# Kernel tuning notes

Hardware: AMD Instinct MI355X
Metric: run time of the kernel (lower is better)

Reference implementation:

```python
import jax, jax.numpy as jnp
import numpy as np

B, T, DIN, DOUT, RANK, UDIM = 4, 2048, 4096, 4096, 2, 16

def setup_inputs() -> dict:
    key = jax.random.key(0)
    ks = jax.random.split(key, 8)
    return {
        "x": jax.random.normal(ks[0], (B, T, DIN), jnp.float32),
        "W": jax.random.normal(ks[1], (DOUT, DIN), jnp.float32) * 0.02,
        "b": jax.random.normal(ks[2], (DOUT,), jnp.float32) * 0.02,
        "U": jax.random.normal(ks[3], (DOUT, RANK), jnp.float32) * 0.02,
        "S": jax.random.normal(ks[4], (RANK, RANK), jnp.float32),
        "Vh": jax.random.normal(ks[5], (RANK, DIN), jnp.float32) * 0.02,
        "P": jax.random.normal(ks[6], (UDIM, RANK, RANK), jnp.float32),
        "v": jax.random.normal(ks[7], (UDIM,), jnp.float32),
    }

def reference(x, W, b, U, S, Vh, P, v):
    # R = sum_u v[u] * P[u]  (intended meaning of einsum('u,urr->rr'))
    R = jnp.einsum('u,uab->ab', v, P)                 # [rank, rank]
    base = jnp.einsum('btd,od->bto', x, W) + b        # frozen linear
    # x @ delta_W.T with delta_W = U @ S @ R @ Vh, chained low-rank:
    M = U @ S @ R                                     # [out, rank]
    t = jnp.einsum('btd,rd->btr', x, Vh)              # [B, T, rank]
    delta = jnp.einsum('btr,or->bto', t, M)           # [B, T, out]
    return base + delta
```

## Files before the change

kernel.cpp:

```cpp
#include <hip/hip_runtime.h>
#include <hip/hip_bf16.h>
#include <stdint.h>

typedef __hip_bfloat16 bf16;
typedef __attribute__((ext_vector_type(8))) short bf16x8;
typedef __attribute__((ext_vector_type(4))) float f32x4;

static constexpr int Mtot = 8192;
static constexpr int Ktot = 4096;
static constexpr int Ntot = 4096;
static constexpr int BM = 256, BN = 256, BK = 64;
static constexpr int NKT = Ktot / BK;
static constexpr int CAST_BLOCKS = (Mtot * Ktot) / 2048;
static constexpr int PREP_BLOCKS = (Ntot * Ktot) / 2048;
static constexpr int WEFF_BLOCKS = Ntot * 2;

__device__ __forceinline__ void gl_lds16(const void* g, void* l) {
  __builtin_amdgcn_global_load_lds(
      (const __attribute__((address_space(1))) void*)g,
      (__attribute__((address_space(3))) void*)l,
      16, 0, 0);
}

__device__ __forceinline__ uint32_t bf16pair(float a, float b) {
  __hip_bfloat16 ha = __float2bfloat16(a), hb = __float2bfloat16(b);
  uint16_t ia, ib;
  __builtin_memcpy(&ia, &ha, 2);
  __builtin_memcpy(&ib, &hb, 2);
  return (uint32_t)ia | ((uint32_t)ib << 16);
}

__global__ __launch_bounds__(256) void mprep_kernel(const float* __restrict__ U,
                                                    const float* __restrict__ S,
                                                    const float* __restrict__ P,
                                                    const float* __restrict__ v,
                                                    float* __restrict__ M) {
  float R0 = 0.f, R1 = 0.f, R2 = 0.f, R3 = 0.f;
#pragma unroll
  for (int u = 0; u < 16; ++u) {
    float vu = v[u];
    R0 += vu * P[u * 4 + 0];
    R1 += vu * P[u * 4 + 1];
    R2 += vu * P[u * 4 + 2];
    R3 += vu * P[u * 4 + 3];
  }
  float SR00 = S[0] * R0 + S[1] * R2, SR01 = S[0] * R1 + S[1] * R3;
  float SR10 = S[2] * R0 + S[3] * R2, SR11 = S[2] * R1 + S[3] * R3;
  const int o = blockIdx.x * 256 + threadIdx.x;
  const float u0 = U[o * 2 + 0], u1 = U[o * 2 + 1];
  ((float2*)M)[o] = make_float2(u0 * SR00 + u1 * SR10, u0 * SR01 + u1 * SR11);
}

__global__ __launch_bounds__(256) void prep_kernel(const float* __restrict__ x,
                                                   bf16* __restrict__ xb,
                                                   const float* __restrict__ W,
                                                   const float* __restrict__ Vh,
                                                   const float* __restrict__ M,
                                                   bf16* __restrict__ Wp) {
  const int bid = blockIdx.x;
  const int t = threadIdx.x;
  if (bid < CAST_BLOCKS) {
    const size_t chunk = (size_t)bid * 2048;
    const float4 a = *(const float4*)(x + chunk + 4 * t);
    const float4 b = *(const float4*)(x + chunk + 1024 + 4 * t);
    uint2 p0, p1;
    p0.x = bf16pair(a.x, a.y); p0.y = bf16pair(a.z, a.w);
    p1.x = bf16pair(b.x, b.y); p1.y = bf16pair(b.z, b.w);
    *(uint2*)(xb + chunk + 4 * t) = p0;
    *(uint2*)(xb + chunk + 1024 + 4 * t) = p1;
  } else {
    const int b2 = bid - CAST_BLOCKS;
    const int o = b2 >> 1;
    const int cb = (b2 & 1) * 2048 + 4 * t;
    const float2 Mo = ((const float2*)M)[o];

    const float* wrow = W + (size_t)o * Ktot;
    const float4 w0 = *(const float4*)(wrow + cb);
    const float4 w1 = *(const float4*)(wrow + cb + 1024);
    const float4 a0 = *(const float4*)(Vh + cb);
    const float4 a1 = *(const float4*)(Vh + cb + 1024);
    const float4 b0 = *(const float4*)(Vh + Ktot + cb);
    const float4 b1 = *(const float4*)(Vh + Ktot + cb + 1024);

    uint2 p0, p1;
    p0.x = bf16pair(w0.x + Mo.x * a0.x + Mo.y * b0.x,
                    w0.y + Mo.x * a0.y + Mo.y * b0.y);
    p0.y = bf16pair(w0.z + Mo.x * a0.z + Mo.y * b0.z,
                    w0.w + Mo.x * a0.w + Mo.y * b0.w);
    p1.x = bf16pair(w1.x + Mo.x * a1.x + Mo.y * b1.x,
                    w1.y + Mo.x * a1.y + Mo.y * b1.y);
    p1.y = bf16pair(w1.z + Mo.x * a1.z + Mo.y * b1.z,
                    w1.w + Mo.x * a1.w + Mo.y * b1.w);
    *(uint2*)(Wp + (size_t)o * Ktot + cb) = p0;
    *(uint2*)(Wp + (size_t)o * Ktot + cb + 1024) = p1;
  }
}


#define SCHEDB __builtin_amdgcn_sched_barrier(0)
#define BAR do { SCHEDB; __builtin_amdgcn_s_barrier(); SCHEDB; } while (0)
#define LG0 do { asm volatile("s_waitcnt lgkmcnt(0)" ::: "memory"); SCHEDB; } while (0)
#define LG8 do { asm volatile("s_waitcnt lgkmcnt(8)" ::: "memory"); } while (0)
#define WVM(n) do { asm volatile("s_waitcnt vmcnt(" #n ")" ::: "memory"); } while (0)

__global__ __launch_bounds__(512, 2) void gemm_kernel(const bf16* __restrict__ A,
                                                      const bf16* __restrict__ Bt,
                                                      const float* __restrict__ bias,
                                                      float* __restrict__ out) {
  __shared__ __align__(16) bf16 As[2][BM * BK];
  __shared__ __align__(16) bf16 Bs[2][BN * BK];

  const int tid = (int)threadIdx.x;
  const int lane = tid & 63;
  const int w = tid >> 6;
  const int wr = w >> 2;
  const int wc = w & 3;

  const int bid = (int)blockIdx.x;
  const int xcd = bid & 7;
  const int ord = bid >> 3;
  const int rnd = ord >> 5;
  const int slt = ord & 31;
  const int mt = rnd * 16 + (xcd >> 1) * 4 + (slt >> 3);
  const int nt = (xcd & 1) * 8 + (slt & 7);
  const int m0 = mt * BM;
  const int n0 = nt * BN;

  const int l8 = lane >> 3;
  const int swcol = ((lane & 7) ^ l8) << 3;
  const bf16* gA = A + (size_t)(m0 + w * 16 + l8) * Ktot + swcol;
  const bf16* gB = Bt + (size_t)(n0 + w * 16 + l8) * Ktot + swcol;

  const int fm = lane & 15;
  const int q = lane >> 4;
  const int rx = (fm & 7) << 4;
  const int clo = (q * 16) ^ (rx & 48);
  const int aoff0 = (wr * 128 + fm) * 128 + clo + (rx & 64);
  const int aoff1 = (wr * 128 + fm) * 128 + clo + (64 ^ (rx & 64));
  const int boff0 = (wc * 64 + fm) * 128 + clo + (rx & 64);
  const int boff1 = (wc * 64 + fm) * 128 + clo + (64 ^ (rx & 64));

#define STA(BUF, half, kt) do { \
    const bf16* _g = gA + (size_t)((half) * 128) * Ktot + (kt) * 64; \
    char* _l = (char*)(&As[BUF][0]) + (half) * 16384 + w * 2048; \
    gl_lds16(_g, _l); \
    gl_lds16(_g + (size_t)8 * Ktot, _l + 1024); \
  } while (0)
#define STB(BUF, half, kt) do { \
    const bf16* _g = gB + (size_t)((half) * 128) * Ktot + (kt) * 64; \
    char* _l = (char*)(&Bs[BUF][0]) + (half) * 16384 + w * 2048; \
    gl_lds16(_g, _l); \
    gl_lds16(_g + (size_t)8 * Ktot, _l + 1024); \
  } while (0)
#define STAGE_H(BUF, h, kt) do { \
    if ((h) == 0) STA(BUF, 0, kt); else if ((h) == 1) STA(BUF, 1, kt); \
    else if ((h) == 2) STB(BUF, 0, kt); else STB(BUF, 1, kt); } while (0)

#define RD_A(dst, BUF, mh) do { \
    const char* _p = (const char*)(&As[BUF][0]) + (mh) * 8192; \
    _Pragma("unroll") for (int _i = 0; _i < 4; ++_i) { \
      dst[_i][0] = *(const bf16x8*)(_p + _i * 2048 + aoff0); \
      dst[_i][1] = *(const bf16x8*)(_p + _i * 2048 + aoff1); \
    } } while (0)
#define RD_B(dst, BUF, nh) do { \
    const char* _p = (const char*)(&Bs[BUF][0]) + (nh) * 4096; \
    _Pragma("unroll") for (int _j = 0; _j < 2; ++_j) { \
      dst[_j][0] = *(const bf16x8*)(_p + _j * 2048 + boff0); \
      dst[_j][1] = *(const bf16x8*)(_p + _j * 2048 + boff1); \
    } } while (0)

#define MFMA_Q(AV, BV, MH, NH) do { \
    __builtin_amdgcn_s_setprio(1); \
    _Pragma("unroll") for (int _i = 0; _i < 4; ++_i) \
    _Pragma("unroll") for (int _j = 0; _j < 2; ++_j) { \
      acc[(MH) * 4 + _i][(NH) * 2 + _j] = __builtin_amdgcn_mfma_f32_16x16x32_bf16( \
          AV[_i][0], BV[_j][0], acc[(MH) * 4 + _i][(NH) * 2 + _j], 0, 0, 0); \
      acc[(MH) * 4 + _i][(NH) * 2 + _j] = __builtin_amdgcn_mfma_f32_16x16x32_bf16( \
          AV[_i][1], BV[_j][1], acc[(MH) * 4 + _i][(NH) * 2 + _j], 0, 0, 0); \
    } \
    __builtin_amdgcn_s_setprio(0); \
  } while (0)

  f32x4 acc[8][4];
#pragma unroll
  for (int i = 0; i < 8; ++i)
#pragma unroll
    for (int j = 0; j < 4; ++j) acc[i][j] = {0.f, 0.f, 0.f, 0.f};

  bf16x8 a[4][2], b0[2][2], b1[2][2];

  STAGE_H(0, 0, 0); STAGE_H(0, 1, 0); STAGE_H(0, 2, 0); STAGE_H(0, 3, 0);
  STAGE_H(1, 2, 1); STAGE_H(1, 3, 1); STAGE_H(1, 0, 1);
  WVM(6);
  BAR;

  for (int it = 0; it < 31; ++it) {
    const int k1 = 2 * it + 1;
    const int k2 = 2 * it + 2;
    const int k3 = 2 * it + 3;
    RD_A(a, 0, 0); RD_B(b0, 0, 0); STAGE_H(1, 1, k1); LG8;
    BAR; LG0; MFMA_Q(a, b0, 0, 0); BAR;
    RD_B(b1, 0, 1);
    BAR; LG0; MFMA_Q(a, b1, 0, 1); BAR;
    RD_A(a, 0, 1); STAGE_H(0, 2, k2);
    BAR; LG0; MFMA_Q(a, b0, 1, 0); BAR;
    STAGE_H(0, 3, k2);
    BAR; MFMA_Q(a, b1, 1, 1); SCHEDB; WVM(4); BAR;
    RD_A(a, 1, 0); RD_B(b0, 1, 0); STAGE_H(0, 0, k2); LG8;
    BAR; LG0; MFMA_Q(a, b0, 0, 0); BAR;
    RD_B(b1, 1, 1); STAGE_H(0, 1, k2);
    BAR; LG0; MFMA_Q(a, b1, 0, 1); BAR;
    RD_A(a, 1, 1); STAGE_H(1, 2, k3);
    BAR; LG0; MFMA_Q(a, b0, 1, 0); BAR;
    STAGE_H(1, 3, k3); STAGE_H(1, 0, k3);
    BAR; MFMA_Q(a, b1, 1, 1); SCHEDB; WVM(6); BAR;
  }

  RD_A(a, 0, 0); RD_B(b0, 0, 0); STAGE_H(1, 1, 63); LG8;
  BAR; LG0; MFMA_Q(a, b0, 0, 0); BAR;
  RD_B(b1, 0, 1);
  BAR; LG0; MFMA_Q(a, b1, 0, 1); BAR;
  RD_A(a, 0, 1);
  BAR; LG0; MFMA_Q(a, b0, 1, 0); BAR;
  BAR; MFMA_Q(a, b1, 1, 1); SCHEDB; WVM(0); BAR;
  RD_A(a, 1, 0); RD_B(b0, 1, 0);
  BAR; LG0; MFMA_Q(a, b0, 0, 0); BAR;
  RD_B(b1, 1, 1);
  BAR; LG0; MFMA_Q(a, b1, 0, 1); BAR;
  RD_A(a, 1, 1);
  BAR; LG0; MFMA_Q(a, b0, 1, 0); BAR;
  MFMA_Q(a, b1, 1, 1);

#pragma unroll
  for (int jb = 0; jb < 4; ++jb) {
    const int gn = n0 + wc * 64 + jb * 16 + fm;
    const float bj = bias[gn];
#pragma unroll
    for (int ia = 0; ia < 8; ++ia) {
      float* o = out + (size_t)(m0 + wr * 128 + ia * 16 + q * 4) * Ntot + gn;
#pragma unroll
      for (int r = 0; r < 4; ++r) o[(size_t)r * Ntot] = acc[ia][jb][r] + bj;
    }
  }

#undef STA
#undef STB
#undef STAGE_H
#undef RD_A
#undef RD_B
#undef MFMA_Q
}

extern "C" void kernel_launch(void* const* d_in, const int* in_sizes, int n_in,
                              void* d_out, int out_size, void* d_ws, size_t ws_size,
                              hipStream_t stream) {
  const float* x  = (const float*)d_in[0];
  const float* W  = (const float*)d_in[1];
  const float* b  = (const float*)d_in[2];
  const float* U  = (const float*)d_in[3];
  const float* S  = (const float*)d_in[4];
  const float* Vh = (const float*)d_in[5];
  const float* P  = (const float*)d_in[6];
  const float* v  = (const float*)d_in[7];
  float* out = (float*)d_out;

  bf16* xb = (bf16*)d_ws;
  bf16* Wp = (bf16*)((char*)d_ws + (size_t)Mtot * Ktot * 2);
  float* M = out;

  mprep_kernel<<<16, 256, 0, stream>>>(U, S, P, v, M);
  prep_kernel<<<CAST_BLOCKS + WEFF_BLOCKS, 256, 0, stream>>>(x, xb, W, Vh, M, Wp);
  gemm_kernel<<<512, 512, 0, stream>>>(xb, Wp, b, out);
}
```

Before: 519.4 us.

## Fuse fp32-to-bf16 cast of x into GEMM A-tile staging

The separate pass that cast x to bf16 in workspace is removed. The GEMM now loads fp32 x tiles into registers, converts them to bf16 and writes them to swizzled LDS, with a reworked software pipeline and waitcnt schedule. This saves the extra global write and read of the bf16 copy of x (about 64MB of traffic). In exchange the GEMM reads twice as many A bytes per tile, A-staging now needs registers and VALU conversion work inside the main loop, and the direct global-to-LDS path is lost for A. The added register pressure could hurt occupancy, and the hand-tuned wait counts must be exactly right.

```diff
diff --git a/kernel.cpp b/kernel.cpp
--- a/kernel.cpp
+++ b/kernel.cpp
@@ -11,8 +11,6 @@
 static constexpr int Ntot = 4096;
 static constexpr int BM = 256, BN = 256, BK = 64;
 static constexpr int NKT = Ktot / BK;
-static constexpr int CAST_BLOCKS = (Mtot * Ktot) / 2048;
-static constexpr int PREP_BLOCKS = (Ntot * Ktot) / 2048;
 static constexpr int WEFF_BLOCKS = Ntot * 2;
 
 __device__ __forceinline__ void gl_lds16(const void* g, void* l) {
@@ -51,59 +49,45 @@
   ((float2*)M)[o] = make_float2(u0 * SR00 + u1 * SR10, u0 * SR01 + u1 * SR11);
 }
 
-__global__ __launch_bounds__(256) void prep_kernel(const float* __restrict__ x,
-                                                   bf16* __restrict__ xb,
-                                                   const float* __restrict__ W,
+__global__ __launch_bounds__(256) void prep_kernel(const float* __restrict__ W,
                                                    const float* __restrict__ Vh,
                                                    const float* __restrict__ M,
                                                    bf16* __restrict__ Wp) {
   const int bid = blockIdx.x;
   const int t = threadIdx.x;
-  if (bid < CAST_BLOCKS) {
-    const size_t chunk = (size_t)bid * 2048;
-    const float4 a = *(const float4*)(x + chunk + 4 * t);
-    const float4 b = *(const float4*)(x + chunk + 1024 + 4 * t);
-    uint2 p0, p1;
-    p0.x = bf16pair(a.x, a.y); p0.y = bf16pair(a.z, a.w);
-    p1.x = bf16pair(b.x, b.y); p1.y = bf16pair(b.z, b.w);
-    *(uint2*)(xb + chunk + 4 * t) = p0;
-    *(uint2*)(xb + chunk + 1024 + 4 * t) = p1;
-  } else {
-    const int b2 = bid - CAST_BLOCKS;
-    const int o = b2 >> 1;
-    const int cb = (b2 & 1) * 2048 + 4 * t;
-    const float2 Mo = ((const float2*)M)[o];
-
-    const float* wrow = W + (size_t)o * Ktot;
-    const float4 w0 = *(const float4*)(wrow + cb);
-    const float4 w1 = *(const float4*)(wrow + cb + 1024);
-    const float4 a0 = *(const float4*)(Vh + cb);
-    const float4 a1 = *(const float4*)(Vh + cb + 1024);
-    const float4 b0 = *(const float4*)(Vh + Ktot + cb);
-    const float4 b1 = *(const float4*)(Vh + Ktot + cb + 1024);
-
-    uint2 p0, p1;
-    p0.x = bf16pair(w0.x + Mo.x * a0.x + Mo.y * b0.x,
-                    w0.y + Mo.x * a0.y + Mo.y * b0.y);
-    p0.y = bf16pair(w0.z + Mo.x * a0.z + Mo.y * b0.z,
-                    w0.w + Mo.x * a0.w + Mo.y * b0.w);
-    p1.x = bf16pair(w1.x + Mo.x * a1.x + Mo.y * b1.x,
-                    w1.y + Mo.x * a1.y + Mo.y * b1.y);
-    p1.y = bf16pair(w1.z + Mo.x * a1.z + Mo.y * b1.z,
-                    w1.w + Mo.x * a1.w + Mo.y * b1.w);
-    *(uint2*)(Wp + (size_t)o * Ktot + cb) = p0;
-    *(uint2*)(Wp + (size_t)o * Ktot + cb + 1024) = p1;
-  }
+  const int o = bid >> 1;
+  const int cb = (bid & 1) * 2048 + 4 * t;
+  const float2 Mo = ((const float2*)M)[o];
+
+  const float* wrow = W + (size_t)o * Ktot;
+  const float4 w0 = *(const float4*)(wrow + cb);
+  const float4 w1 = *(const float4*)(wrow + cb + 1024);
+  const float4 a0 = *(const float4*)(Vh + cb);
+  const float4 a1 = *(const float4*)(Vh + cb + 1024);
+  const float4 b0 = *(const float4*)(Vh + Ktot + cb);
+  const float4 b1 = *(const float4*)(Vh + Ktot + cb + 1024);
+
+  uint2 p0, p1;
+  p0.x = bf16pair(w0.x + Mo.x * a0.x + Mo.y * b0.x,
+                  w0.y + Mo.x * a0.y + Mo.y * b0.y);
+  p0.y = bf16pair(w0.z + Mo.x * a0.z + Mo.y * b0.z,
+                  w0.w + Mo.x * a0.w + Mo.y * b0.w);
+  p1.x = bf16pair(w1.x + Mo.x * a1.x + Mo.y * b1.x,
+                  w1.y + Mo.x * a1.y + Mo.y * b1.y);
+  p1.y = bf16pair(w1.z + Mo.x * a1.z + Mo.y * b1.z,
+                  w1.w + Mo.x * a1.w + Mo.y * b1.w);
+  *(uint2*)(Wp + (size_t)o * Ktot + cb) = p0;
+  *(uint2*)(Wp + (size_t)o * Ktot + cb + 1024) = p1;
 }
 
 
 #define SCHEDB __builtin_amdgcn_sched_barrier(0)
 #define BAR do { SCHEDB; __builtin_amdgcn_s_barrier(); SCHEDB; } while (0)
 #define LG0 do { asm volatile("s_waitcnt lgkmcnt(0)" ::: "memory"); SCHEDB; } while (0)
-#define LG8 do { asm volatile("s_waitcnt lgkmcnt(8)" ::: "memory"); } while (0)
+#define LGN(n) do { asm volatile("s_waitcnt lgkmcnt(" #n ")" ::: "memory"); } while (0)
 #define WVM(n) do { asm volatile("s_waitcnt vmcnt(" #n ")" ::: "memory"); } while (0)
 
-__global__ __launch_bounds__(512, 2) void gemm_kernel(const bf16* __restrict__ A,
+__global__ __launch_bounds__(512, 2) void gemm_kernel(const float* __restrict__ x,
                                                       const bf16* __restrict__ Bt,
                                                       const float* __restrict__ bias,
                                                       float* __restrict__ out) {
@@ -128,8 +112,15 @@
 
   const int l8 = lane >> 3;
   const int swcol = ((lane & 7) ^ l8) << 3;
-  const bf16* gA = A + (size_t)(m0 + w * 16 + l8) * Ktot + swcol;
   const bf16* gB = Bt + (size_t)(n0 + w * 16 + l8) * Ktot + swcol;
+
+  const int ar = tid >> 2;
+  const int ac = (tid & 3) << 4;
+  const float* gAx = x + (size_t)(m0 + ar) * Ktot + ac;
+  const int c0 = (tid & 3) << 5;
+  const int asw = (ar & 7) << 4;
+  const int aw0 = ar * 128 + (c0 ^ asw);
+  const int aw1 = ar * 128 + ((c0 + 16) ^ asw);
 
   const int fm = lane & 15;
   const int q = lane >> 4;
@@ -140,11 +131,33 @@
   const int boff0 = (wc * 64 + fm) * 128 + clo + (rx & 64);
   const int boff1 = (wc * 64 + fm) * 128 + clo + (64 ^ (rx & 64));
 
-#define STA(BUF, half, kt) do { \
-    const bf16* _g = gA + (size_t)((half) * 128) * Ktot + (kt) * 64; \
-    char* _l = (char*)(&As[BUF][0]) + (half) * 16384 + w * 2048; \
-    gl_lds16(_g, _l); \
-    gl_lds16(_g + (size_t)8 * Ktot, _l + 1024); \
+#define IA0(ub, kt) do { \
+    const float* _g = gAx + (size_t)((ub) * 128) * Ktot + (kt) * 64; \
+    sA0[0] = *(const float4*)(_g + 0);  sA0[1] = *(const float4*)(_g + 4); \
+    sA0[2] = *(const float4*)(_g + 8);  sA0[3] = *(const float4*)(_g + 12); \
+  } while (0)
+#define IA1(ub, kt) do { \
+    const float* _g = gAx + (size_t)((ub) * 128) * Ktot + (kt) * 64; \
+    sA1[0] = *(const float4*)(_g + 0);  sA1[1] = *(const float4*)(_g + 4); \
+    sA1[2] = *(const float4*)(_g + 8);  sA1[3] = *(const float4*)(_g + 12); \
+  } while (0)
+#define WRA0(BUF, ub) do { \
+    char* _b = (char*)(&As[BUF][0]) + (ub) * 16384; \
+    uint4 _lo, _hi; \
+    _lo.x = bf16pair(sA0[0].x, sA0[0].y); _lo.y = bf16pair(sA0[0].z, sA0[0].w); \
+    _lo.z = bf16pair(sA0[1].x, sA0[1].y); _lo.w = bf16pair(sA0[1].z, sA0[1].w); \
+    _hi.x = bf16pair(sA0[2].x, sA0[2].y); _hi.y = bf16pair(sA0[2].z, sA0[2].w); \
+    _hi.z = bf16pair(sA0[3].x, sA0[3].y); _hi.w = bf16pair(sA0[3].z, sA0[3].w); \
+    *(uint4*)(_b + aw0) = _lo; *(uint4*)(_b + aw1) = _hi; \
+  } while (0)
+#define WRA1(BUF, ub) do { \
+    char* _b = (char*)(&As[BUF][0]) + (ub) * 16384; \
+    uint4 _lo, _hi; \
+    _lo.x = bf16pair(sA1[0].x, sA1[0].y); _lo.y = bf16pair(sA1[0].z, sA1[0].w); \
+    _lo.z = bf16pair(sA1[1].x, sA1[1].y); _lo.w = bf16pair(sA1[1].z, sA1[1].w); \
+    _hi.x = bf16pair(sA1[2].x, sA1[2].y); _hi.y = bf16pair(sA1[2].z, sA1[2].w); \
+    _hi.z = bf16pair(sA1[3].x, sA1[3].y); _hi.w = bf16pair(sA1[3].z, sA1[3].w); \
+    *(uint4*)(_b + aw0) = _lo; *(uint4*)(_b + aw1) = _hi; \
   } while (0)
 #define STB(BUF, half, kt) do { \
     const bf16* _g = gB + (size_t)((half) * 128) * Ktot + (kt) * 64; \
@@ -152,9 +165,6 @@
     gl_lds16(_g, _l); \
     gl_lds16(_g + (size_t)8 * Ktot, _l + 1024); \
   } while (0)
-#define STAGE_H(BUF, h, kt) do { \
-    if ((h) == 0) STA(BUF, 0, kt); else if ((h) == 1) STA(BUF, 1, kt); \
-    else if ((h) == 2) STB(BUF, 0, kt); else STB(BUF, 1, kt); } while (0)
 
 #define RD_A(dst, BUF, mh) do { \
     const char* _p = (const char*)(&As[BUF][0]) + (mh) * 8192; \
@@ -188,36 +198,50 @@
     for (int j = 0; j < 4; ++j) acc[i][j] = {0.f, 0.f, 0.f, 0.f};
 
   bf16x8 a[4][2], b0[2][2], b1[2][2];
-
-  STAGE_H(0, 0, 0); STAGE_H(0, 1, 0); STAGE_H(0, 2, 0); STAGE_H(0, 3, 0);
-  STAGE_H(1, 2, 1); STAGE_H(1, 3, 1); STAGE_H(1, 0, 1);
-  WVM(6);
+  float4 sA0[4], sA1[4];
+
+  IA0(0, 0); IA1(1, 0);
+  STB(0, 0, 0); STB(0, 1, 0);
+  WVM(8);  WRA0(0, 0);
+  WVM(4);  WRA1(0, 1);
+  IA0(0, 1);
+  WVM(0);  WRA0(1, 0);
+  IA1(1, 1);
+  STB(1, 0, 1); STB(1, 1, 1);
+  LGN(0);
   BAR;
 
   for (int it = 0; it < 31; ++it) {
-    const int k1 = 2 * it + 1;
     const int k2 = 2 * it + 2;
     const int k3 = 2 * it + 3;
-    RD_A(a, 0, 0); RD_B(b0, 0, 0); STAGE_H(1, 1, k1); LG8;
-    BAR; LG0; MFMA_Q(a, b0, 0, 0); BAR;
+    WVM(4); WRA1(1, 1);
+    RD_A(a, 0, 0); RD_B(b0, 0, 0);
+    LGN(12); BAR; LG0; MFMA_Q(a, b0, 0, 0); BAR;
     RD_B(b1, 0, 1);
     BAR; LG0; MFMA_Q(a, b1, 0, 1); BAR;
-    RD_A(a, 0, 1); STAGE_H(0, 2, k2);
+    IA0(0, k2); STB(0, 0, k2);
+    RD_A(a, 0, 1);
     BAR; LG0; MFMA_Q(a, b0, 1, 0); BAR;
-    STAGE_H(0, 3, k2);
-    BAR; MFMA_Q(a, b1, 1, 1); SCHEDB; WVM(4); BAR;
-    RD_A(a, 1, 0); RD_B(b0, 1, 0); STAGE_H(0, 0, k2); LG8;
-    BAR; LG0; MFMA_Q(a, b0, 0, 0); BAR;
-    RD_B(b1, 1, 1); STAGE_H(0, 1, k2);
-    BAR; LG0; MFMA_Q(a, b1, 0, 1); BAR;
-    RD_A(a, 1, 1); STAGE_H(1, 2, k3);
+    IA1(1, k2); STB(0, 1, k2);
+    BAR; MFMA_Q(a, b1, 1, 1); SCHEDB; WVM(12); BAR;
+    WVM(8); WRA0(0, 0);
+    RD_A(a, 1, 0); RD_B(b0, 1, 0);
+    LGN(12); BAR; LG0; MFMA_Q(a, b0, 0, 0); BAR;
+    IA0(0, k3);
+    WVM(6); WRA1(0, 1);
+    RD_B(b1, 1, 1);
+    LGN(4); BAR; LG0; MFMA_Q(a, b1, 0, 1); BAR;
+    IA1(1, k3); STB(1, 0, k3);
+    RD_A(a, 1, 1);
     BAR; LG0; MFMA_Q(a, b0, 1, 0); BAR;
-    STAGE_H(1, 3, k3); STAGE_H(1, 0, k3);
-    BAR; MFMA_Q(a, b1, 1, 1); SCHEDB; WVM(6); BAR;
+    STB(1, 1, k3);
+    WVM(8); WRA0(1, 0);
+    LGN(0); BAR; MFMA_Q(a, b1, 1, 1); BAR;
   }
 
-  RD_A(a, 0, 0); RD_B(b0, 0, 0); STAGE_H(1, 1, 63); LG8;
-  BAR; LG0; MFMA_Q(a, b0, 0, 0); BAR;
+  WVM(4); WRA1(1, 1);
+  RD_A(a, 0, 0); RD_B(b0, 0, 0);
+  LGN(12); BAR; LG0; MFMA_Q(a, b0, 0, 0); BAR;
   RD_B(b1, 0, 1);
   BAR; LG0; MFMA_Q(a, b1, 0, 1); BAR;
   RD_A(a, 0, 1);
@@ -243,9 +267,11 @@
     }
   }
 
-#undef STA
+#undef IA0
+#undef IA1
+#undef WRA0
+#undef WRA1
 #undef STB
-#undef STAGE_H
 #undef RD_A
 #undef RD_B
 #undef MFMA_Q
@@ -264,11 +290,10 @@
   const float* v  = (const float*)d_in[7];
   float* out = (float*)d_out;
 
-  bf16* xb = (bf16*)d_ws;
-  bf16* Wp = (bf16*)((char*)d_ws + (size_t)Mtot * Ktot * 2);
+  bf16* Wp = (bf16*)d_ws;
   float* M = out;
 
   mprep_kernel<<<16, 256, 0, stream>>>(U, S, P, v, M);
-  prep_kernel<<<CAST_BLOCKS + WEFF_BLOCKS, 256, 0, stream>>>(x, xb, W, Vh, M, Wp);
-  gemm_kernel<<<512, 512, 0, stream>>>(xb, Wp, b, out);
-}
+  prep_kernel<<<WEFF_BLOCKS, 256, 0, stream>>>(W, Vh, M, Wp);
+  gemm_kernel<<<512, 512, 0, stream>>>(x, Wp, b, out);
+}
```

Result: slower. 671.5 us (+29.3%).

## Prefetch LDS fragments earlier with a second A register set and partial lgkmcnt waits

Applied to the files above, without the earlier changes.

Reschedules the LDS-to-register fragment reads in the GEMM main loop. B fragments for both column halves are read together, and the second A fragment goes into a new register buffer a2 while the earlier MFMAs run. Waits become partial (lgkmcnt 4/8) instead of full drains. The goal is to hide LDS read latency behind MFMA work. The extra 32 VGPRs for a2 may cause spills at the 512x2 launch bound, and the hand-counted lgkmcnt values must match the actual number of outstanding LDS ops.

```diff
diff --git a/kernel.cpp b/kernel.cpp
--- a/kernel.cpp
+++ b/kernel.cpp
@@ -12,7 +12,6 @@
 static constexpr int BM = 256, BN = 256, BK = 64;
 static constexpr int NKT = Ktot / BK;
 static constexpr int CAST_BLOCKS = (Mtot * Ktot) / 2048;
-static constexpr int PREP_BLOCKS = (Ntot * Ktot) / 2048;
 static constexpr int WEFF_BLOCKS = Ntot * 2;
 
 __device__ __forceinline__ void gl_lds16(const void* g, void* l) {
@@ -99,8 +98,8 @@
 
 #define SCHEDB __builtin_amdgcn_sched_barrier(0)
 #define BAR do { SCHEDB; __builtin_amdgcn_s_barrier(); SCHEDB; } while (0)
-#define LG0 do { asm volatile("s_waitcnt lgkmcnt(0)" ::: "memory"); SCHEDB; } while (0)
-#define LG8 do { asm volatile("s_waitcnt lgkmcnt(8)" ::: "memory"); } while (0)
+#define LGW(n) do { asm volatile("s_waitcnt lgkmcnt(" #n ")" ::: "memory"); SCHEDB; } while (0)
+#define LGP(n) do { asm volatile("s_waitcnt lgkmcnt(" #n ")" ::: "memory"); } while (0)
 #define WVM(n) do { asm volatile("s_waitcnt vmcnt(" #n ")" ::: "memory"); } while (0)
 
 __global__ __launch_bounds__(512, 2) void gemm_kernel(const bf16* __restrict__ A,
@@ -187,7 +186,7 @@
 #pragma unroll
     for (int j = 0; j < 4; ++j) acc[i][j] = {0.f, 0.f, 0.f, 0.f};
 
-  bf16x8 a[4][2], b0[2][2], b1[2][2];
+  bf16x8 a[4][2], a2[4][2], b0[2][2], b1[2][2];
 
   STAGE_H(0, 0, 0); STAGE_H(0, 1, 0); STAGE_H(0, 2, 0); STAGE_H(0, 3, 0);
   STAGE_H(1, 2, 1); STAGE_H(1, 3, 1); STAGE_H(1, 0, 1);
@@ -198,38 +197,36 @@
     const int k1 = 2 * it + 1;
     const int k2 = 2 * it + 2;
     const int k3 = 2 * it + 3;
-    RD_A(a, 0, 0); RD_B(b0, 0, 0); STAGE_H(1, 1, k1); LG8;
-    BAR; LG0; MFMA_Q(a, b0, 0, 0); BAR;
-    RD_B(b1, 0, 1);
-    BAR; LG0; MFMA_Q(a, b1, 0, 1); BAR;
-    RD_A(a, 0, 1); STAGE_H(0, 2, k2);
-    BAR; LG0; MFMA_Q(a, b0, 1, 0); BAR;
+    RD_A(a, 0, 0); RD_B(b0, 0, 0); RD_B(b1, 0, 1); STAGE_H(1, 1, k1); LGP(8);
+    BAR; LGW(4); MFMA_Q(a, b0, 0, 0); BAR;
+    RD_A(a2, 0, 1);
+    BAR; LGW(8); MFMA_Q(a, b1, 0, 1); BAR;
+    STAGE_H(0, 2, k2);
+    BAR; LGW(0); MFMA_Q(a2, b0, 1, 0); BAR;
     STAGE_H(0, 3, k2);
-    BAR; MFMA_Q(a, b1, 1, 1); SCHEDB; WVM(4); BAR;
-    RD_A(a, 1, 0); RD_B(b0, 1, 0); STAGE_H(0, 0, k2); LG8;
-    BAR; LG0; MFMA_Q(a, b0, 0, 0); BAR;
-    RD_B(b1, 1, 1); STAGE_H(0, 1, k2);
-    BAR; LG0; MFMA_Q(a, b1, 0, 1); BAR;
-    RD_A(a, 1, 1); STAGE_H(1, 2, k3);
-    BAR; LG0; MFMA_Q(a, b0, 1, 0); BAR;
+    BAR; MFMA_Q(a2, b1, 1, 1); SCHEDB; WVM(4); BAR;
+    RD_A(a, 1, 0); RD_B(b0, 1, 0); RD_B(b1, 1, 1); STAGE_H(0, 0, k2); LGP(8);
+    BAR; LGW(4); MFMA_Q(a, b0, 0, 0); BAR;
+    RD_A(a2, 1, 1); STAGE_H(0, 1, k2);
+    BAR; LGW(8); MFMA_Q(a, b1, 0, 1); BAR;
+    STAGE_H(1, 2, k3);
+    BAR; LGW(0); MFMA_Q(a2, b0, 1, 0); BAR;
     STAGE_H(1, 3, k3); STAGE_H(1, 0, k3);
-    BAR; MFMA_Q(a, b1, 1, 1); SCHEDB; WVM(6); BAR;
-  }
-
-  RD_A(a, 0, 0); RD_B(b0, 0, 0); STAGE_H(1, 1, 63); LG8;
-  BAR; LG0; MFMA_Q(a, b0, 0, 0); BAR;
-  RD_B(b1, 0, 1);
-  BAR; LG0; MFMA_Q(a, b1, 0, 1); BAR;
-  RD_A(a, 0, 1);
-  BAR; LG0; MFMA_Q(a, b0, 1, 0); BAR;
-  BAR; MFMA_Q(a, b1, 1, 1); SCHEDB; WVM(0); BAR;
-  RD_A(a, 1, 0); RD_B(b0, 1, 0);
-  BAR; LG0; MFMA_Q(a, b0, 0, 0); BAR;
-  RD_B(b1, 1, 1);
-  BAR; LG0; MFMA_Q(a, b1, 0, 1); BAR;
-  RD_A(a, 1, 1);
-  BAR; LG0; MFMA_Q(a, b0, 1, 0); BAR;
-  MFMA_Q(a, b1, 1, 1);
+    BAR; MFMA_Q(a2, b1, 1, 1); SCHEDB; WVM(6); BAR;
+  }
+
+  RD_A(a, 0, 0); RD_B(b0, 0, 0); RD_B(b1, 0, 1); STAGE_H(1, 1, 63); LGP(8);
+  BAR; LGW(4); MFMA_Q(a, b0, 0, 0); BAR;
+  RD_A(a2, 0, 1);
+  BAR; LGW(8); MFMA_Q(a, b1, 0, 1); BAR;
+  BAR; LGW(0); MFMA_Q(a2, b0, 1, 0); BAR;
+  BAR; MFMA_Q(a2, b1, 1, 1); SCHEDB; WVM(0); BAR;
+  RD_A(a, 1, 0); RD_B(b0, 1, 0); RD_B(b1, 1, 1); LGP(8);
+  BAR; LGW(4); MFMA_Q(a, b0, 0, 0); BAR;
+  RD_A(a2, 1, 1);
+  BAR; LGW(8); MFMA_Q(a, b1, 0, 1); BAR;
+  BAR; LGW(0); MFMA_Q(a2, b0, 1, 0); BAR;
+  MFMA_Q(a2, b1, 1, 1);
 
 #pragma unroll
   for (int jb = 0; jb < 4; ++jb) {
```

After: 511.2 us. No clear change (-1.6%).
